# Optimization experiments

Hardware: AMD Instinct MI355X
Metric: run time of the kernel (lower is better)

The kernel has to match this reference:

```python
import jax, jax.numpy as jnp
import numpy as np

GROUP = 64          # quantization group size (axis=0 grouping)
IN_F = 4096
OUT_F = 11008
N_GROUPS = IN_F * OUT_F // GROUP  # 704512


def setup_inputs() -> dict:
    key = jax.random.key(0)
    k0, k1, k2, k3, k4 = jax.random.split(key, 5)
    x = jax.random.normal(k0, (4, 2048, IN_F), dtype=jnp.float32)
    # packed 4-bit codes: two codes per byte, rows 0..31 hold high nibbles,
    # unpacked rows 32..63 come from low nibbles (HQQ pack_4bit_u8 layout)
    W_q = jax.random.randint(k1, (GROUP // 2, N_GROUPS), 0, 256, dtype=jnp.int32)
    # scale here is meta['scale'] = 1/quant_scale, i.e. the dequant multiplier
    scale = jax.random.uniform(k2, (1, N_GROUPS), dtype=jnp.float32) * 0.01 + 1e-4
    zero = jax.random.uniform(k3, (1, N_GROUPS), dtype=jnp.float32) * 15.0
    bias = jax.random.normal(k4, (OUT_F,), dtype=jnp.float32) * 0.01
    return {"x": x, "W_q": W_q, "scale": scale, "zero": zero, "bias": bias}


def _dequantize(W_q, scale, zero):
    # unpack_4bit_u8: high nibble -> first half of rows, low nibble -> second half
    high = (W_q >> 4) & 0xF
    low = W_q & 0xF
    W_r = jnp.concatenate([high, low], axis=0).astype(jnp.float32)  # [64, N_GROUPS]
    W = (W_r - zero) * scale                                        # affine dequant
    return W.reshape(OUT_F, IN_F)


def reference(x, W_q, scale, zero, bias):
    W = _dequantize(W_q, scale, zero)          # [out, in]
    out = jnp.einsum('bsi,oi->bso', x, W)      # x @ W.T
    return out + bias
```

## Files before the change

kernel.cpp:

```cpp
#include <hip/hip_runtime.h>


#define K_DIM 4096
#define N_DIM 11008
#define M_DIM 8192
#define NG 704512

#define BM 256
#define BN 256
#define BK 64
#define NKT 64
#define NIT 32

typedef __bf16 bf16;
typedef bf16 bf16x4 __attribute__((ext_vector_type(4)));
typedef bf16 bf16x8 __attribute__((ext_vector_type(8)));
typedef float f32x4 __attribute__((ext_vector_type(4)));

__device__ __forceinline__ void async_copy16(const void* g, void* l) {
  __builtin_amdgcn_global_load_lds(
      (const __attribute__((address_space(1))) void*)g,
      (__attribute__((address_space(3))) void*)l,
      16, 0, 0);
}

__device__ __forceinline__ void barrier_() {
  asm volatile("" ::: "memory");
  __builtin_amdgcn_s_barrier();
  asm volatile("" ::: "memory");
}
#define VMW(n) asm volatile("s_waitcnt vmcnt(" #n ")" ::: "memory")

__global__ void cvt_x(const float* __restrict__ X, bf16* __restrict__ Xb) {
  const int idx = (blockIdx.x * 256 + threadIdx.x) * 4;
  const float4 v = *(const float4*)(X + idx);
  bf16x4 o;
  o[0] = (bf16)v.x; o[1] = (bf16)v.y; o[2] = (bf16)v.z; o[3] = (bf16)v.w;
  *(bf16x4*)(Xb + idx) = o;
}

__global__ void dequant_w(const int* __restrict__ Wq, const float* __restrict__ scale,
                          const float* __restrict__ zero, bf16* __restrict__ Wb) {
  const int idx = blockIdx.x * 256 + threadIdx.x;
  const int r = idx / (NG / 4);
  const int g = (idx - r * (NG / 4)) * 4;
  const int4 q = *(const int4*)(Wq + r * NG + g);
  const float4 sc = *(const float4*)(scale + g);
  const float4 zp = *(const float4*)(zero + g);
  const int c = g >> 12;
  const int i = g & 4095;
  bf16x4 hi, lo;
  hi[0] = (bf16)(((float)((q.x >> 4) & 0xF) - zp.x) * sc.x);
  hi[1] = (bf16)(((float)((q.y >> 4) & 0xF) - zp.y) * sc.y);
  hi[2] = (bf16)(((float)((q.z >> 4) & 0xF) - zp.z) * sc.z);
  hi[3] = (bf16)(((float)((q.w >> 4) & 0xF) - zp.w) * sc.w);
  lo[0] = (bf16)(((float)(q.x & 0xF) - zp.x) * sc.x);
  lo[1] = (bf16)(((float)(q.y & 0xF) - zp.y) * sc.y);
  lo[2] = (bf16)(((float)(q.z & 0xF) - zp.z) * sc.z);
  lo[3] = (bf16)(((float)(q.w & 0xF) - zp.w) * sc.w);
  *(bf16x4*)(Wb + (size_t)(r * 172 + c) * 4096 + i) = hi;
  *(bf16x4*)(Wb + (size_t)((r + 32) * 172 + c) * 4096 + i) = lo;
}

__global__ __launch_bounds__(512, 2)
void gemm_bt(const bf16* __restrict__ A, const bf16* __restrict__ B,
             const float* __restrict__ bias, float* __restrict__ C) {
  extern __shared__ char smem[];

  const int tid = threadIdx.x;
  const int wave = tid >> 6;
  const int lane = tid & 63;
  const int l15 = lane & 15;
  const int quad = lane >> 4;
  const int wm = wave >> 2;
  const int wn = wave & 3;

  const int id = blockIdx.x;
  const int wg = (id & 7) * 172 + (id >> 3);
  const int bm = (wg & 31) * BM;
  const int bn = (wg >> 5) * BN;

  const int srow = tid >> 3;
  const int qc = (tid & 7) ^ (srow & 7);
  const bf16* sA = A + (size_t)(bm + srow) * K_DIM + qc * 8;
  const bf16* sB = B + (size_t)(bn + srow) * K_DIM + qc * 8;
  const int ldsWave = wave << 10;

  auto stageA = [&](int b, int h, int t) {
    const bf16* g = sA + (size_t)(h * 128) * K_DIM + (size_t)t * BK;
    char* l = smem + (b * 2 + h) * 16384 + ldsWave;
    async_copy16(g, l);
    async_copy16(g + (size_t)64 * K_DIM, l + 8192);
  };
  auto stageB = [&](int b, int h, int t) {
    const bf16* g = sB + (size_t)(h * 128) * K_DIM + (size_t)t * BK;
    char* l = smem + 65536 + (b * 2 + h) * 16384 + ldsWave;
    async_copy16(g, l);
    async_copy16(g + (size_t)64 * K_DIM, l + 8192);
  };

  const int sw = l15 & 7;
  const int ro = l15 * 128;
  const int k0 = (quad ^ sw) << 4;
  const int k1 = ((quad + 4) ^ sw) << 4;
  const char* rdA0 = smem + wm * 16384 + ro;
  const char* rdB0 = smem + 65536 + (wn >> 1) * 16384 + (wn & 1) * 8192 + ro;

  auto ldA = [&](bf16x8 (&d)[4][2], const char* base, int fm) {
#pragma unroll
    for (int m = 0; m < 4; ++m) {
      const char* p = base + (fm + m) * 2048;
      d[m][0] = *(const bf16x8*)(p + k0);
      d[m][1] = *(const bf16x8*)(p + k1);
    }
  };
  auto ldB = [&](bf16x8 (&d)[2][2], const char* base, int gn) {
#pragma unroll
    for (int n = 0; n < 2; ++n) {
      const char* p = base + (gn + n) * 2048;
      d[n][0] = *(const bf16x8*)(p + k0);
      d[n][1] = *(const bf16x8*)(p + k1);
    }
  };

  f32x4 acc[8][4];
#pragma unroll
  for (int m = 0; m < 8; ++m)
#pragma unroll
    for (int n = 0; n < 4; ++n) {
      f32x4 z = {0.f, 0.f, 0.f, 0.f};
      acc[m][n] = z;
    }

  auto mmq = [&](bf16x8 (&a)[4][2], bf16x8 (&b)[2][2], int fm, int gn) {
    __builtin_amdgcn_s_setprio(1);
#pragma unroll
    for (int m = 0; m < 4; ++m)
#pragma unroll
      for (int n = 0; n < 2; ++n) {
        acc[fm + m][gn + n] = __builtin_amdgcn_mfma_f32_16x16x32_bf16(
            a[m][0], b[n][0], acc[fm + m][gn + n], 0, 0, 0);
        acc[fm + m][gn + n] = __builtin_amdgcn_mfma_f32_16x16x32_bf16(
            a[m][1], b[n][1], acc[fm + m][gn + n], 0, 0, 0);
      }
    __builtin_amdgcn_s_setprio(0);
    __builtin_amdgcn_sched_barrier(0);
  };

  stageA(0, 0, 0); stageA(0, 1, 0); stageB(0, 0, 0); stageB(0, 1, 0);
  stageA(1, 0, 1);
  VMW(2);
  barrier_();

  for (int it = 0; it < NIT; ++it) {
    const int t1 = 2 * it + 1, t2 = 2 * it + 2, t3 = 2 * it + 3;
    const bool more = (it < NIT - 1);
    bf16x8 a0[4][2], a1[4][2], p0[2][2], p1[2][2];

    ldA(a0, rdA0, 0); ldB(p0, rdB0, 0);
    stageA(1, 1, t1);
    barrier_(); mmq(a0, p0, 0, 0); barrier_();
    ldB(p1, rdB0, 2);
    stageB(1, 0, t1);
    barrier_(); mmq(a0, p1, 0, 2); barrier_();
    ldA(a1, rdA0, 4);
    stageB(1, 1, t1);
    barrier_(); mmq(a1, p0, 4, 0); barrier_();
    if (more) { stageA(0, 0, t2); VMW(2); } else { VMW(0); }
    barrier_(); mmq(a1, p1, 4, 2); barrier_();

    const char* rA = rdA0 + 32768;
    const char* rB = rdB0 + 32768;
    ldA(a0, rA, 0); ldB(p0, rB, 0);
    if (more) stageA(0, 1, t2);
    barrier_(); mmq(a0, p0, 0, 0); barrier_();
    ldB(p1, rB, 2);
    if (more) stageB(0, 0, t2);
    barrier_(); mmq(a0, p1, 0, 2); barrier_();
    ldA(a1, rA, 4);
    if (more) stageB(0, 1, t2);
    barrier_(); mmq(a1, p0, 4, 0); barrier_();
    if (more) { stageA(1, 0, t3); VMW(2); }
    barrier_(); mmq(a1, p1, 4, 2); barrier_();
  }

  const int cm = bm + wm * 128 + quad * 4;
  const int cn = bn + wn * 64 + l15;
#pragma unroll
  for (int g = 0; g < 4; ++g) {
    const int col = cn + g * 16;
    const float bv = bias[col];
#pragma unroll
    for (int m = 0; m < 8; ++m) {
      float* cp = C + (size_t)(cm + m * 16) * N_DIM + col;
      const f32x4 a = acc[m][g];
      __builtin_nontemporal_store(a[0] + bv, cp + 0 * N_DIM);
      __builtin_nontemporal_store(a[1] + bv, cp + 1 * N_DIM);
      __builtin_nontemporal_store(a[2] + bv, cp + 2 * N_DIM);
      __builtin_nontemporal_store(a[3] + bv, cp + 3 * N_DIM);
    }
  }
}

extern "C" void kernel_launch(void* const* d_in, const int* in_sizes, int n_in,
                              void* d_out, int out_size, void* d_ws, size_t ws_size,
                              hipStream_t stream) {
  const float* x = (const float*)d_in[0];
  const int* Wq = (const int*)d_in[1];
  const float* scale = (const float*)d_in[2];
  const float* zero = (const float*)d_in[3];
  const float* bias = (const float*)d_in[4];
  float* out = (float*)d_out;

  bf16* Xb = (bf16*)d_ws;
  bf16* Wb = (bf16*)((char*)d_ws + (size_t)67108864);

  static int smem_set = 0;
  if (!smem_set) {
    (void)hipFuncSetAttribute((const void*)gemm_bt,
                              hipFuncAttributeMaxDynamicSharedMemorySize, 131072);
    smem_set = 1;
  }

  cvt_x<<<32768, 256, 0, stream>>>(x, Xb);
  dequant_w<<<22016, 256, 0, stream>>>(Wq, scale, zero, Wb);
  gemm_bt<<<1376, 512, 131072, stream>>>(Xb, Wb, bias, out);
}
```

Measured before the change: 1.207 ms.

## Overlap LDS fragment loads with MFMA by software-pipelining register reads

Restructures the GEMM main loop so LDS reads for the next MFMA block are issued before the current MFMA block runs, instead of between barriers with nothing to hide behind. The initial fragment loads are hoisted out of the loop and the next half-tile's loads are prefetched at the end of each phase. The order of global-to-LDS staging also changes: B tiles are prefetched a stage ahead and the vmcnt waits are adjusted. This overlaps LDS latency with matrix-core work, at the cost of more live registers and a more delicate barrier and hazard ordering.

```diff
diff --git a/kernel.cpp b/kernel.cpp
--- a/kernel.cpp
+++ b/kernel.cpp
@@ -105,6 +105,8 @@
   const int k1 = ((quad + 4) ^ sw) << 4;
   const char* rdA0 = smem + wm * 16384 + ro;
   const char* rdB0 = smem + 65536 + (wn >> 1) * 16384 + (wn & 1) * 8192 + ro;
+  const char* rdA1 = rdA0 + 32768;
+  const char* rdB1 = rdB0 + 32768;
 
   auto ldA = [&](bf16x8 (&d)[4][2], const char* base, int fm) {
 #pragma unroll
@@ -147,41 +149,56 @@
     __builtin_amdgcn_sched_barrier(0);
   };
 
-  stageA(0, 0, 0); stageA(0, 1, 0); stageB(0, 0, 0); stageB(0, 1, 0);
-  stageA(1, 0, 1);
-  VMW(2);
+  bf16x8 a0[4][2], a1[4][2], p0[2][2], p1[2][2];
+
+  stageB(0, 0, 0); stageB(0, 1, 0); stageA(0, 0, 0); stageA(0, 1, 0);
+  stageB(1, 0, 1); stageB(1, 1, 1);
+  VMW(4);
   barrier_();
+  ldA(a0, rdA0, 0); ldB(p0, rdB0, 0);
 
   for (int it = 0; it < NIT; ++it) {
     const int t1 = 2 * it + 1, t2 = 2 * it + 2, t3 = 2 * it + 3;
     const bool more = (it < NIT - 1);
-    bf16x8 a0[4][2], a1[4][2], p0[2][2], p1[2][2];
-
-    ldA(a0, rdA0, 0); ldB(p0, rdB0, 0);
+
+    stageA(1, 0, t1);
+    barrier_();
+    ldB(p1, rdB0, 2);
+    mmq(a0, p0, 0, 0);
+    barrier_();
     stageA(1, 1, t1);
-    barrier_(); mmq(a0, p0, 0, 0); barrier_();
-    ldB(p1, rdB0, 2);
-    stageB(1, 0, t1);
-    barrier_(); mmq(a0, p1, 0, 2); barrier_();
+    barrier_();
     ldA(a1, rdA0, 4);
-    stageB(1, 1, t1);
-    barrier_(); mmq(a1, p0, 4, 0); barrier_();
-    if (more) { stageA(0, 0, t2); VMW(2); } else { VMW(0); }
-    barrier_(); mmq(a1, p1, 4, 2); barrier_();
-
-    const char* rA = rdA0 + 32768;
-    const char* rB = rdB0 + 32768;
-    ldA(a0, rA, 0); ldB(p0, rB, 0);
+    mmq(a0, p1, 0, 2);
+    barrier_();
+    if (more) stageB(0, 0, t2);
+    barrier_();
+    mmq(a1, p0, 4, 0);
+    barrier_();
+    if (more) { stageB(0, 1, t2); VMW(4); } else { VMW(0); }
+    barrier_();
+    ldA(a0, rdA1, 0); ldB(p0, rdB1, 0);
+    mmq(a1, p1, 4, 2);
+    barrier_();
+    if (more) stageA(0, 0, t2);
+    barrier_();
+    ldB(p1, rdB1, 2);
+    mmq(a0, p0, 0, 0);
+    barrier_();
     if (more) stageA(0, 1, t2);
-    barrier_(); mmq(a0, p0, 0, 0); barrier_();
-    ldB(p1, rB, 2);
-    if (more) stageB(0, 0, t2);
-    barrier_(); mmq(a0, p1, 0, 2); barrier_();
-    ldA(a1, rA, 4);
-    if (more) stageB(0, 1, t2);
-    barrier_(); mmq(a1, p0, 4, 0); barrier_();
-    if (more) { stageA(1, 0, t3); VMW(2); }
-    barrier_(); mmq(a1, p1, 4, 2); barrier_();
+    barrier_();
+    ldA(a1, rdA1, 4);
+    mmq(a0, p1, 0, 2);
+    barrier_();
+    if (more) stageB(1, 0, t3);
+    barrier_();
+    mmq(a1, p0, 4, 0);
+    barrier_();
+    if (more) { stageB(1, 1, t3); VMW(4); }
+    barrier_();
+    if (more) { ldA(a0, rdA0, 0); ldB(p0, rdB0, 0); }
+    mmq(a1, p1, 4, 2);
+    barrier_();
   }
 
   const int cm = bm + wm * 128 + quad * 4;
```

New measurement: 1.070 ms. -11.4%, faster.
